# Kernel tuning notes

Hardware: AMD Instinct MI355X
Metric: run time of the kernel (lower is better)

## Reference

```python
import jax, jax.numpy as jnp
import numpy as np

B, S = 4, 4096
D_MODEL = 1024
INDEXER_DIM = 64
LOCAL_WINDOW = 16
MEDIUM_WINDOW = 64
GLOBAL_K = 32
LOCAL_SPARSE = 0.8


def _local_k_schedule(seq_len):
    # Replicates torch: k_local = max(1, int(L * (1 - local_sparse))) with Python float math
    ks = []
    for q in range(seq_len):
        L = min(q + 1, LOCAL_WINDOW)
        ks.append(max(1, int(L * (1.0 - LOCAL_SPARSE))))
    ks = np.asarray(ks, dtype=np.int32)
    return ks, int(ks.max())


def setup_inputs() -> dict:
    key = jax.random.key(0)
    kx, kl, km, kg = jax.random.split(key, 4)
    scale = D_MODEL ** -0.5
    return {
        "x": jax.random.normal(kx, (B, S, D_MODEL), jnp.float32),
        "W_local": jax.random.normal(kl, (INDEXER_DIM, D_MODEL), jnp.float32) * scale,
        "W_medium": jax.random.normal(km, (INDEXER_DIM, D_MODEL), jnp.float32) * scale,
        "W_global": jax.random.normal(kg, (INDEXER_DIM, D_MODEL), jnp.float32) * scale,
    }


def reference(x, W_local, W_medium, W_global):
    Bb, Ss, _ = x.shape
    neg_inf = jnp.array(-jnp.inf, x.dtype)
    zero = jnp.array(0.0, x.dtype)

    lf = x @ W_local.T   # [B,S,i]
    mf = x @ W_medium.T  # computed by the original but DEAD: medium branch never fires
    gf = x @ W_global.T  # [B,S,i]

    mask = jnp.full((Bb, 1, Ss, Ss), -jnp.inf, x.dtype)
    q_ix = jnp.arange(Ss)
    b_ix = jnp.arange(Bb)[:, None, None]
    qq = q_ix[None, :, None]

    # ---- local scale: causal window [max(0, q-W+1), q] ----
    offs = jnp.arange(LOCAL_WINDOW)
    win = q_ix[:, None] - (LOCAL_WINDOW - 1) + offs[None, :]  # [S,W] absolute key positions
    valid = win >= 0
    winc = jnp.clip(win, 0, Ss - 1)
    lwin = lf[:, winc]                                        # [B,S,W,i]
    lscores = jax.nn.relu(jnp.einsum('bqd,bqwd->bqw', lf, lwin))
    lscores = jnp.where(valid[None], lscores, -jnp.inf)
    ks, kmax = _local_k_schedule(Ss)
    _, tl = jax.lax.top_k(lscores, kmax)                      # [B,S,kmax] window-relative
    labs = jnp.take_along_axis(jnp.broadcast_to(winc[None], (Bb, Ss, LOCAL_WINDOW)), tl, axis=-1)
    keep = jnp.arange(kmax)[None, None, :] < jnp.asarray(ks)[None, :, None]  # [1,S,kmax]
    lvals = jnp.where(keep, zero, neg_inf)
    mask = mask.at[b_ix, 0, qq, labs].max(jnp.broadcast_to(lvals, labs.shape))

    # ---- medium scale: DEAD CODE in the original (medium_end == local_end always) ----

    # ---- global scale (active because seq_len > medium_window and global_k > 0) ----
    if Ss > MEDIUM_WINDOW and GLOBAL_K > 0:
        gs = jax.nn.relu(jnp.einsum('bqd,bkd->bqk', gf, gf))  # [B,S,S]
        j = jnp.arange(Ss)[None, :]
        banned = (j <= q_ix[:, None]) & (j >= q_ix[:, None] - (LOCAL_WINDOW - 1))  # [S,S]
        gs = jnp.where(banned[None], -jnp.inf, gs)
        _, tg = jax.lax.top_k(gs, GLOBAL_K)                   # [B,S,Kg]
        mask = mask.at[b_ix, 0, qq, tg].max(jnp.zeros(tg.shape, x.dtype))

    return mask
```

## Files before the change

### kernel.cpp

```cpp
#include <hip/hip_runtime.h>
#include <hip/hip_fp16.h>
#include <cstdint>

#define SEQ 4096
#define NB 4
#define DMODEL 1024
#define ID 64
#define LW 16
#define GK 32
#define TQ 4

#define NEG_INF (-__builtin_inff())
#define MASKED4 0xFBFFFBFFu

__device__ __forceinline__ float2 h2f2(unsigned int u) {
    __half2 h = *reinterpret_cast<__half2*>(&u);
    return __half22float2(h);
}

__global__ __launch_bounds__(256)
void hp_feat_v7(const unsigned short* __restrict__ x,
                const unsigned short* __restrict__ Wl,
                const unsigned short* __restrict__ Wg,
                float* __restrict__ lf, float* __restrict__ gfT)
{
    __shared__ float xs[32][68];
    __shared__ float ws[32][68];
    __shared__ float trans[64][68];

    const int tid = threadIdx.x;
    const int half = blockIdx.x & 1;
    const long row0 = (long)(blockIdx.x >> 1) * 64;
    const unsigned short* W = half ? Wg : Wl;
    const int tx = tid & 15, ty = tid >> 4;

    float acc[4][4];
#pragma unroll
    for (int r = 0; r < 4; r++)
#pragma unroll
        for (int c = 0; c < 4; c++) acc[r][c] = 0.f;

    for (int k0 = 0; k0 < DMODEL; k0 += 32) {
        {
            int r = tid >> 2, c8 = (tid & 3) * 8;
            uint4 v = *(const uint4*)(x + (row0 + r) * DMODEL + k0 + c8);
            float2 f;
            f = h2f2(v.x); xs[c8 + 0][r] = f.x; xs[c8 + 1][r] = f.y;
            f = h2f2(v.y); xs[c8 + 2][r] = f.x; xs[c8 + 3][r] = f.y;
            f = h2f2(v.z); xs[c8 + 4][r] = f.x; xs[c8 + 5][r] = f.y;
            f = h2f2(v.w); xs[c8 + 6][r] = f.x; xs[c8 + 7][r] = f.y;
        }
        {
            int r = tid >> 2, c8 = (tid & 3) * 8;
            uint4 v = *(const uint4*)(W + (long)r * DMODEL + k0 + c8);
            float2 f;
            f = h2f2(v.x); ws[c8 + 0][r] = f.x; ws[c8 + 1][r] = f.y;
            f = h2f2(v.y); ws[c8 + 2][r] = f.x; ws[c8 + 3][r] = f.y;
            f = h2f2(v.z); ws[c8 + 4][r] = f.x; ws[c8 + 5][r] = f.y;
            f = h2f2(v.w); ws[c8 + 6][r] = f.x; ws[c8 + 7][r] = f.y;
        }
        __syncthreads();
#pragma unroll
        for (int kk = 0; kk < 32; kk++) {
            float4 a  = *(const float4*)&xs[kk][ty * 4];
            float4 bv = *(const float4*)&ws[kk][tx * 4];
            const float ar[4] = {a.x, a.y, a.z, a.w};
            const float bc[4] = {bv.x, bv.y, bv.z, bv.w};
#pragma unroll
            for (int r = 0; r < 4; r++)
#pragma unroll
                for (int c = 0; c < 4; c++)
                    acc[r][c] = fmaf(ar[r], bc[c], acc[r][c]);
        }
        __syncthreads();
    }

    if (!half) {
#pragma unroll
        for (int r = 0; r < 4; r++) {
            float4 st = make_float4(acc[r][0], acc[r][1], acc[r][2], acc[r][3]);
            *(float4*)(lf + (row0 + ty * 4 + r) * ID + tx * 4) = st;
        }
    } else {
#pragma unroll
        for (int r = 0; r < 4; r++)
#pragma unroll
            for (int c = 0; c < 4; c++)
                trans[tx * 4 + c][ty * 4 + r] = acc[r][c];
        __syncthreads();
        const int b = (int)(row0 >> 12), s0 = (int)(row0 & 4095);
        const int col = tid >> 2, rs = (tid & 3) * 16;
        float* dst = gfT + ((long)b * ID + col) * SEQ + s0 + rs;
#pragma unroll
        for (int u = 0; u < 4; u++)
            *(float4*)(dst + 4 * u) = *(const float4*)&trans[col][rs + 4 * u];
    }
}

__global__ __launch_bounds__(256)
void hp_mask_v8(const float* __restrict__ lf, const float* __restrict__ gfT,
                unsigned short* __restrict__ out)
{
    __shared__ float qv[TQ][ID];
    __shared__ float lq[TQ][ID];
    __shared__ unsigned long long red[4][4];
    __shared__ unsigned int bitmap[TQ][SEQ / 32];
    __shared__ float lsc[TQ][LW];
    __shared__ unsigned short tm[256];

    const int tid = threadIdx.x;
    const int lane = tid & 63, w = tid >> 6;
    const int bq = blockIdx.x;
    const int b = bq >> 10;
    const int q0 = (bq & 1023) * TQ;
    const float* gTb = gfT + (long)b * ID * SEQ;
    const float* lfb = lf + (long)b * SEQ * ID;

    {
        int d = tid >> 2, qi = tid & 3;
        qv[qi][d] = gTb[(long)d * SEQ + q0 + qi];
        int qi2 = tid >> 6, d2 = tid & 63;
        lq[qi2][d2] = lfb[(long)(q0 + qi2) * ID + d2];
        ((unsigned int*)bitmap)[tid] = 0u;
        ((unsigned int*)bitmap)[tid + 256] = 0u;
    }
    __syncthreads();

    float acc[4][4][TQ];
#pragma unroll
    for (int c = 0; c < 4; c++)
#pragma unroll
        for (int j = 0; j < 4; j++)
#pragma unroll
            for (int qi = 0; qi < TQ; qi++) acc[c][j][qi] = 0.f;

    for (int d = 0; d < ID; d++) {
        float qd[TQ];
#pragma unroll
        for (int qi = 0; qi < TQ; qi++) qd[qi] = qv[qi][d];
        const float4* rowp = (const float4*)(gTb + (long)d * SEQ);
#pragma unroll
        for (int c = 0; c < 4; c++) {
            float4 kv = rowp[c * 256 + tid];
#pragma unroll
            for (int qi = 0; qi < TQ; qi++) {
                acc[c][0][qi] = fmaf(kv.x, qd[qi], acc[c][0][qi]);
                acc[c][1][qi] = fmaf(kv.y, qd[qi], acc[c][1][qi]);
                acc[c][2][qi] = fmaf(kv.z, qd[qi], acc[c][2][qi]);
                acc[c][3][qi] = fmaf(kv.w, qd[qi], acc[c][3][qi]);
            }
        }
    }

    unsigned int uv[4][4][TQ];
#pragma unroll
    for (int c = 0; c < 4; c++)
#pragma unroll
        for (int j = 0; j < 4; j++) {
            const int k = 1024 * c + 4 * tid + j;
#pragma unroll
            for (int qi = 0; qi < TQ; qi++) {
                const int q = q0 + qi;
                const bool banned = (k <= q) && (k >= q - (LW - 1));
                uv[c][j][qi] = banned ? 0u
                    : (__float_as_uint(fmaxf(acc[c][j][qi], 0.f)) + 1u);
            }
        }

    unsigned int lo[TQ], hi[TQ];
#pragma unroll
    for (int qi = 0; qi < TQ; qi++) { lo[qi] = 0u; hi[qi] = 0xFFFFFFFFu; }

#pragma unroll 1
    for (int it = 0; it < 32; ++it) {
        unsigned int mid[TQ];
        unsigned long long pc = 0ull;
#pragma unroll
        for (int qi = 0; qi < TQ; qi++) {
            mid[qi] = lo[qi] + ((hi[qi] - lo[qi]) >> 1);
            int cnt = 0;
#pragma unroll
            for (int c = 0; c < 4; c++)
#pragma unroll
                for (int j = 0; j < 4; j++)
                    cnt += __popcll(__ballot(uv[c][j][qi] >= mid[qi]));
            pc |= (unsigned long long)(unsigned int)cnt << (16 * qi);
        }
        if (lane == 0) red[it & 1][w] = pc;
        __syncthreads();
        const unsigned long long tot = red[it & 1][0] + red[it & 1][1]
                                     + red[it & 1][2] + red[it & 1][3];
#pragma unroll
        for (int qi = 0; qi < TQ; qi++) {
            const unsigned int cnt =
                (unsigned int)((tot >> (16 * qi)) & 0xFFFFull);
            if (cnt >= GK) lo[qi] = mid[qi]; else hi[qi] = mid[qi];
        }
    }

    int C1[TQ], T[TQ], need[TQ];
    {
        unsigned long long pg = 0ull, pe = 0ull;
#pragma unroll
        for (int qi = 0; qi < TQ; qi++) {
            int cg = 0, ce = 0;
#pragma unroll
            for (int c = 0; c < 4; c++)
#pragma unroll
                for (int j = 0; j < 4; j++) {
                    const unsigned int v = uv[c][j][qi];
                    cg += __popcll(__ballot(v > lo[qi]));
                    ce += __popcll(__ballot(v == lo[qi]));
                }
            pg |= (unsigned long long)(unsigned int)cg << (16 * qi);
            pe |= (unsigned long long)(unsigned int)ce << (16 * qi);
        }
        if (lane == 0) { red[2][w] = pg; red[3][w] = pe; }
        __syncthreads();
        const unsigned long long tg = red[2][0] + red[2][1] + red[2][2] + red[2][3];
        const unsigned long long te = red[3][0] + red[3][1] + red[3][2] + red[3][3];
#pragma unroll
        for (int qi = 0; qi < TQ; qi++) {
            C1[qi]   = (int)((tg >> (16 * qi)) & 0xFFFFull);
            T[qi]    = (int)((te >> (16 * qi)) & 0xFFFFull);
            need[qi] = GK - C1[qi];
        }
    }

#pragma unroll
    for (int qi = 0; qi < TQ; qi++) {
        const bool allties = (T[qi] == need[qi]);
#pragma unroll
        for (int c = 0; c < 4; c++)
#pragma unroll
            for (int j = 0; j < 4; j++) {
                const unsigned int v = uv[c][j][qi];
                const bool sel_ = (v > lo[qi]) | (allties & (v == lo[qi]));
                if (sel_) {
                    const int k = 1024 * c + 4 * tid + j;
                    atomicOr(&bitmap[qi][k >> 5], 1u << (k & 31));
                }
            }
    }

#pragma unroll 1
    for (int qi = 0; qi < TQ; qi++) {
        if (T[qi] > need[qi]) {
            unsigned int m16 = 0u;
#pragma unroll
            for (int c = 0; c < 4; c++)
#pragma unroll
                for (int j = 0; j < 4; j++)
                    if (uv[c][j][qi] == lo[qi]) m16 |= 1u << (c * 4 + j);
            tm[tid] = (unsigned short)m16;
            __syncthreads();
            if (tid == 0) {
                int taken = 0;
                for (int c = 0; c < 4 && taken < need[qi]; c++)
                    for (int t = 0; t < 256 && taken < need[qi]; t++) {
                        const unsigned int nib = ((unsigned int)tm[t] >> (c * 4)) & 15u;
                        for (int j = 0; j < 4 && taken < need[qi]; j++)
                            if ((nib >> j) & 1u) {
                                const int k = 1024 * c + 4 * t + j;
                                atomicOr(&bitmap[qi][k >> 5], 1u << (k & 31));
                                taken++;
                            }
                    }
            }
            __syncthreads();
        }
    }

    if (tid < TQ * LW) {
        int qi = tid >> 4, wnd = tid & 15;
        int q = q0 + qi;
        int win = q - (LW - 1) + wnd;
        float v = NEG_INF;
        if (win >= 0) {
            const float4* kr = (const float4*)(lfb + (long)win * ID);
            float s = 0.f;
#pragma unroll
            for (int d = 0; d < 16; d++) {
                float4 kvv = kr[d];
                const float4 qd = *(const float4*)&lq[qi][d * 4];
                s = fmaf(kvv.x, qd.x, s); s = fmaf(kvv.y, qd.y, s);
                s = fmaf(kvv.z, qd.z, s); s = fmaf(kvv.w, qd.w, s);
            }
            v = fmaxf(s, 0.f);
        }
        lsc[qi][wnd] = v;
    }
    __syncthreads();
    if (tid < TQ) {
        int qi = tid, q = q0 + qi;
        int L = (q + 1 < LW) ? q + 1 : LW;
        int ks = L / 5; if (ks < 1) ks = 1;
        for (int t = 0; t < ks; t++) {
            float best = NEG_INF; int bi = 0;
            for (int wnd = 0; wnd < LW; wnd++) {
                float v = lsc[qi][wnd];
                if (v > best) { best = v; bi = wnd; }
            }
            lsc[qi][bi] = NEG_INF;
            const int win = q - (LW - 1) + bi;
            atomicOr(&bitmap[qi][win >> 5], 1u << (win & 31));
        }
    }
    __syncthreads();

    uint4* orow = (uint4*)(out + ((long)b * SEQ + q0) * SEQ);
#pragma unroll
    for (int i = 0; i < TQ * SEQ / 8 / 256; i++) {
        const int li = i * 256 + tid;
        const int qi = li >> 9;
        const int w8 = li & 511;
        const unsigned int bits =
            (bitmap[qi][w8 >> 2] >> ((w8 & 3) * 8)) & 0xFFu;
        uint4 v;
        v.x = MASKED4 & ~(((bits &   1u) ? 0x0000FFFFu : 0u) |
                          ((bits &   2u) ? 0xFFFF0000u : 0u));
        v.y = MASKED4 & ~(((bits &   4u) ? 0x0000FFFFu : 0u) |
                          ((bits &   8u) ? 0xFFFF0000u : 0u));
        v.z = MASKED4 & ~(((bits &  16u) ? 0x0000FFFFu : 0u) |
                          ((bits &  32u) ? 0xFFFF0000u : 0u));
        v.w = MASKED4 & ~(((bits &  64u) ? 0x0000FFFFu : 0u) |
                          ((bits & 128u) ? 0xFFFF0000u : 0u));
        orow[li] = v;
    }
}

extern "C" void kernel_launch(void* const* d_in, const int* in_sizes, int n_in,
                              void* d_out, int out_size, void* d_ws, size_t ws_size,
                              hipStream_t stream) {
    const unsigned short* x  = (const unsigned short*)d_in[0];
    const unsigned short* Wl = (const unsigned short*)d_in[1];
    const unsigned short* Wg = (const unsigned short*)d_in[3];
    unsigned short* out = (unsigned short*)d_out;

    float* lf  = (float*)d_ws;
    float* gfT = lf + (long)NB * SEQ * ID;

    hp_feat_v7<<<(NB * SEQ / 64) * 2, 256, 0, stream>>>(x, Wl, Wg, lf, gfT);
    hp_mask_v8<<<NB * SEQ / TQ, 256, 0, stream>>>(lf, gfT, out);
}
```

Baseline: 758.6 us.

## Split-K the feature GEMM, add reduce kernel, float-domain top-k search with early exit

The feature projection kernel is split along the model dimension into up to four partial products, chosen by workspace size, and a new reduce kernel sums them, so the small 512-block launch can fill more of the GPU. The mask kernel stops building a separate unsigned-key register array. It now bisects directly on float thresholds held in the accumulator registers and leaves the 32-step search early once every query's interval has converged. The cost is an extra kernel launch plus extra workspace traffic for the partial sums, and a changed float summation order in the features.

Result: slower. 789.6 us (+4.1%).

```diff
diff --git a/kernel.cpp b/kernel.cpp
--- a/kernel.cpp
+++ b/kernel.cpp
@@ -12,6 +12,7 @@
 
 #define NEG_INF (-__builtin_inff())
 #define MASKED4 0xFBFFFBFFu
+#define FMAT (NB * SEQ * ID)
 
 __device__ __forceinline__ float2 h2f2(unsigned int u) {
     __half2 h = *reinterpret_cast<__half2*>(&u);
@@ -19,20 +20,26 @@
 }
 
 __global__ __launch_bounds__(256)
-void hp_feat_v7(const unsigned short* __restrict__ x,
+void hp_feat_v9(const unsigned short* __restrict__ x,
                 const unsigned short* __restrict__ Wl,
                 const unsigned short* __restrict__ Wg,
-                float* __restrict__ lf, float* __restrict__ gfT)
+                float* __restrict__ plf, float* __restrict__ pgf,
+                int ksplit)
 {
-    __shared__ float xs[32][68];
-    __shared__ float ws[32][68];
-    __shared__ float trans[64][68];
+    __shared__ float pool[2 * 32 * 68];
+    float (*xs)[68] = (float(*)[68])pool;
+    float (*ws)[68] = (float(*)[68])(pool + 32 * 68);
+    float (*trans)[68] = (float(*)[68])pool;
 
     const int tid = threadIdx.x;
-    const int half = blockIdx.x & 1;
-    const long row0 = (long)(blockIdx.x >> 1) * 64;
+    const int rest = blockIdx.x & 511;
+    const int kp = blockIdx.x >> 9;
+    const int half = rest & 1;
+    const long row0 = (long)(rest >> 1) * 64;
     const unsigned short* W = half ? Wg : Wl;
     const int tx = tid & 15, ty = tid >> 4;
+    const int kw = DMODEL / ksplit;
+    const int kbase = kp * kw;
 
     float acc[4][4];
 #pragma unroll
@@ -40,7 +47,7 @@
 #pragma unroll
         for (int c = 0; c < 4; c++) acc[r][c] = 0.f;
 
-    for (int k0 = 0; k0 < DMODEL; k0 += 32) {
+    for (int k0 = kbase; k0 < kbase + kw; k0 += 32) {
         {
             int r = tid >> 2, c8 = (tid & 3) * 8;
             uint4 v = *(const uint4*)(x + (row0 + r) * DMODEL + k0 + c8);
@@ -75,11 +82,13 @@
         __syncthreads();
     }
 
+    float* lfp = plf + (long)kp * FMAT;
+    float* gfp = pgf + (long)kp * FMAT;
     if (!half) {
 #pragma unroll
         for (int r = 0; r < 4; r++) {
             float4 st = make_float4(acc[r][0], acc[r][1], acc[r][2], acc[r][3]);
-            *(float4*)(lf + (row0 + ty * 4 + r) * ID + tx * 4) = st;
+            *(float4*)(lfp + (row0 + ty * 4 + r) * ID + tx * 4) = st;
         }
     } else {
 #pragma unroll
@@ -90,7 +99,7 @@
         __syncthreads();
         const int b = (int)(row0 >> 12), s0 = (int)(row0 & 4095);
         const int col = tid >> 2, rs = (tid & 3) * 16;
-        float* dst = gfT + ((long)b * ID + col) * SEQ + s0 + rs;
+        float* dst = gfp + ((long)b * ID + col) * SEQ + s0 + rs;
 #pragma unroll
         for (int u = 0; u < 4; u++)
             *(float4*)(dst + 4 * u) = *(const float4*)&trans[col][rs + 4 * u];
@@ -98,7 +107,24 @@
 }
 
 __global__ __launch_bounds__(256)
-void hp_mask_v8(const float* __restrict__ lf, const float* __restrict__ gfT,
+void hp_reduce(float4* __restrict__ ws4, int ksplit)
+{
+    const int M = FMAT / 4;
+    const int i = blockIdx.x * 256 + threadIdx.x;
+    const int ingf = i >= M;
+    const long base = ingf ? (long)ksplit * M : 0;
+    const int j = ingf ? i - M : i;
+    float4 s = ws4[base + j];
+#pragma unroll 1
+    for (int p = 1; p < ksplit; p++) {
+        float4 v = ws4[base + j + (long)p * M];
+        s.x += v.x; s.y += v.y; s.z += v.z; s.w += v.w;
+    }
+    ws4[base + j] = s;
+}
+
+__global__ __launch_bounds__(256)
+void hp_mask_v9(const float* __restrict__ lf, const float* __restrict__ gfT,
                 unsigned short* __restrict__ out)
 {
     __shared__ float qv[TQ][ID];
@@ -152,7 +178,6 @@
         }
     }
 
-    unsigned int uv[4][4][TQ];
 #pragma unroll
     for (int c = 0; c < 4; c++)
 #pragma unroll
@@ -162,14 +187,13 @@
             for (int qi = 0; qi < TQ; qi++) {
                 const int q = q0 + qi;
                 const bool banned = (k <= q) && (k >= q - (LW - 1));
-                uv[c][j][qi] = banned ? 0u
-                    : (__float_as_uint(fmaxf(acc[c][j][qi], 0.f)) + 1u);
+                acc[c][j][qi] = banned ? -1.0f : fmaxf(acc[c][j][qi], 0.f);
             }
         }
 
     unsigned int lo[TQ], hi[TQ];
 #pragma unroll
-    for (int qi = 0; qi < TQ; qi++) { lo[qi] = 0u; hi[qi] = 0xFFFFFFFFu; }
+    for (int qi = 0; qi < TQ; qi++) { lo[qi] = 0u; hi[qi] = 0x7F800000u; }
 
 #pragma unroll 1
     for (int it = 0; it < 32; ++it) {
@@ -178,24 +202,28 @@
 #pragma unroll
         for (int qi = 0; qi < TQ; qi++) {
             mid[qi] = lo[qi] + ((hi[qi] - lo[qi]) >> 1);
+            const float tf = __uint_as_float(mid[qi] - 1u);
             int cnt = 0;
 #pragma unroll
             for (int c = 0; c < 4; c++)
 #pragma unroll
                 for (int j = 0; j < 4; j++)
-                    cnt += __popcll(__ballot(uv[c][j][qi] >= mid[qi]));
+                    cnt += __popcll(__ballot(acc[c][j][qi] >= tf));
             pc |= (unsigned long long)(unsigned int)cnt << (16 * qi);
         }
         if (lane == 0) red[it & 1][w] = pc;
         __syncthreads();
         const unsigned long long tot = red[it & 1][0] + red[it & 1][1]
                                      + red[it & 1][2] + red[it & 1][3];
+        int conv = 1;
 #pragma unroll
         for (int qi = 0; qi < TQ; qi++) {
             const unsigned int cnt =
                 (unsigned int)((tot >> (16 * qi)) & 0xFFFFull);
             if (cnt >= GK) lo[qi] = mid[qi]; else hi[qi] = mid[qi];
-        }
+            conv &= (hi[qi] - lo[qi] <= 1u);
+        }
+        if (conv) break;
     }
 
     int C1[TQ], T[TQ], need[TQ];
@@ -203,14 +231,16 @@
         unsigned long long pg = 0ull, pe = 0ull;
 #pragma unroll
         for (int qi = 0; qi < TQ; qi++) {
+            const float tg = __uint_as_float(lo[qi]);
+            const unsigned int eb = lo[qi] - 1u;
             int cg = 0, ce = 0;
 #pragma unroll
             for (int c = 0; c < 4; c++)
 #pragma unroll
                 for (int j = 0; j < 4; j++) {
-                    const unsigned int v = uv[c][j][qi];
-                    cg += __popcll(__ballot(v > lo[qi]));
-                    ce += __popcll(__ballot(v == lo[qi]));
+                    const float v = acc[c][j][qi];
+                    cg += __popcll(__ballot(v >= tg));
+                    ce += __popcll(__ballot(__float_as_uint(v) == eb));
                 }
             pg |= (unsigned long long)(unsigned int)cg << (16 * qi);
             pe |= (unsigned long long)(unsigned int)ce << (16 * qi);
@@ -230,12 +260,15 @@
 #pragma unroll
     for (int qi = 0; qi < TQ; qi++) {
         const bool allties = (T[qi] == need[qi]);
+        const float tg = __uint_as_float(lo[qi]);
+        const unsigned int eb = lo[qi] - 1u;
 #pragma unroll
         for (int c = 0; c < 4; c++)
 #pragma unroll
             for (int j = 0; j < 4; j++) {
-                const unsigned int v = uv[c][j][qi];
-                const bool sel_ = (v > lo[qi]) | (allties & (v == lo[qi]));
+                const float v = acc[c][j][qi];
+                const bool sel_ = (v >= tg)
+                                | (allties & (__float_as_uint(v) == eb));
                 if (sel_) {
                     const int k = 1024 * c + 4 * tid + j;
                     atomicOr(&bitmap[qi][k >> 5], 1u << (k & 31));
@@ -246,12 +279,14 @@
 #pragma unroll 1
     for (int qi = 0; qi < TQ; qi++) {
         if (T[qi] > need[qi]) {
+            const unsigned int eb = lo[qi] - 1u;
             unsigned int m16 = 0u;
 #pragma unroll
             for (int c = 0; c < 4; c++)
 #pragma unroll
                 for (int j = 0; j < 4; j++)
-                    if (uv[c][j][qi] == lo[qi]) m16 |= 1u << (c * 4 + j);
+                    if (__float_as_uint(acc[c][j][qi]) == eb)
+                        m16 |= 1u << (c * 4 + j);
             tm[tid] = (unsigned short)m16;
             __syncthreads();
             if (tid == 0) {
@@ -337,9 +372,16 @@
     const unsigned short* Wg = (const unsigned short*)d_in[3];
     unsigned short* out = (unsigned short*)d_out;
 
-    float* lf  = (float*)d_ws;
-    float* gfT = lf + (long)NB * SEQ * ID;
-
-    hp_feat_v7<<<(NB * SEQ / 64) * 2, 256, 0, stream>>>(x, Wl, Wg, lf, gfT);
-    hp_mask_v8<<<NB * SEQ / TQ, 256, 0, stream>>>(lf, gfT, out);
-}
+    const size_t MB4 = (size_t)FMAT * sizeof(float);
+    int ksplit = 1;
+    if (ws_size >= 8 * MB4)      ksplit = 4;
+    else if (ws_size >= 4 * MB4) ksplit = 2;
+
+    float* plf = (float*)d_ws;
+    float* pgf = plf + (long)ksplit * FMAT;
+
+    hp_feat_v9<<<512 * ksplit, 256, 0, stream>>>(x, Wl, Wg, plf, pgf, ksplit);
+    if (ksplit > 1)
+        hp_reduce<<<2 * FMAT / 4 / 256, 256, 0, stream>>>((float4*)d_ws, ksplit);
+    hp_mask_v9<<<NB * SEQ / TQ, 256, 0, stream>>>(plf, pgf, out);
+}
```
